# Kernel tuning notes

Measured on AMD Instinct MI355X. Metric: run time of the kernel, lower is better.

Reference implementation:

```python
import jax, jax.numpy as jnp
import numpy as np

B, L, HSIZE = 16, 512, 1024
H, D = 16, 64  # HHEAD = HSIZE/base, HBASE = 64

def setup_inputs() -> dict:
    key = jax.random.key(0)
    ks = jax.random.split(key, 10)
    inp = {
        'v': jax.random.normal(ks[0], (B, L, HSIZE), jnp.float32),
        'k': jax.random.normal(ks[1], (B, L, HSIZE), jnp.float32),
        'q': jax.random.normal(ks[2], (B, L, HSIZE), jnp.float32),
        'img_abs': jax.random.normal(ks[3], (B, L, HSIZE), jnp.float32),
        'Wv': jax.random.normal(ks[4], (HSIZE, HSIZE), jnp.float32) * 0.02,
        'Wk': jax.random.normal(ks[5], (HSIZE, HSIZE), jnp.float32) * 0.02,
        'Wq': jax.random.normal(ks[6], (HSIZE, HSIZE), jnp.float32) * 0.02,
        'Wm': jax.random.normal(ks[7], (HSIZE, HSIZE), jnp.float32) * 0.02,
        'abs_mask': jax.random.bernoulli(ks[8], 0.1, (B, 1, L, L)),
        'mask': jax.random.bernoulli(ks[9], 0.1, (B, 1, L, L)),
    }
    return inp

def reference(v, k, q, img_abs, Wv, Wk, Wq, Wm, abs_mask, mask):
    nb = q.shape[0]
    # Linear (no bias) then split heads: [B, L, HSIZE] -> [B, H, L, D]
    def heads(x):
        return x.reshape(nb, -1, H, D).transpose(0, 2, 1, 3)
    vh = heads(v @ Wv.T)
    kh = heads(k @ Wk.T)
    qh = heads(q @ Wq.T)
    ph = heads(img_abs)
    scale = 1.0 / jnp.sqrt(jnp.asarray(D, qh.dtype))
    # modulate: attention of q over positional features, residual-added to q
    s1 = jnp.einsum('bhqd,bhpd->bhqp', qh, ph) * scale
    s1 = jnp.where(abs_mask, jnp.asarray(-1e9, s1.dtype), s1)
    qh = qh + jnp.einsum('bhqp,bhpd->bhqd', jax.nn.softmax(s1, axis=-1), ph)
    # main attention (dropout = identity in eval mode)
    s2 = jnp.einsum('bhqd,bhkd->bhqk', qh, kh) * scale
    s2 = jnp.where(mask, jnp.asarray(-1e9, s2.dtype), s2)
    atted = jnp.einsum('bhqk,bhkd->bhqd', jax.nn.softmax(s2, axis=-1), vh)
    atted = atted.transpose(0, 2, 1, 3).reshape(nb, -1, H * D)
    return atted @ Wm.T
```

## Files before the change

kernel.cpp:

```cpp
#include <hip/hip_runtime.h>

typedef unsigned short u16;
typedef unsigned int u32;
typedef unsigned long long u64;
typedef __attribute__((ext_vector_type(8))) short short8;
typedef __attribute__((ext_vector_type(4))) float f32x4;
typedef __attribute__((ext_vector_type(4))) u32 u32x4;

#define NB 16
#define SL 512
#define HS 1024
#define NHEAD 16
#define HD 64
#define NTOKC (16L * 512 * 1024)
#define NWC   (1024L * 1024)
#define NMC   (16L * 512 * 512)

typedef const __attribute__((address_space(1))) u32* gas_t;
typedef __attribute__((address_space(3))) u32* las_t;

__device__ __forceinline__ void gld16(const u16* g, u16* l) {
  __builtin_amdgcn_global_load_lds((gas_t)g, (las_t)l, 16, 0, 0);
}

__device__ __forceinline__ u16 f2bf(float f) {
  union { float f; unsigned u; } c; c.f = f;
  unsigned r = c.u + 0x7FFFu + ((c.u >> 16) & 1u);
  return (u16)(r >> 16);
}
__device__ __forceinline__ float bf2f(u16 u) {
  union { float f; unsigned u; } c; c.u = ((unsigned)u) << 16;
  return c.f;
}

__global__ __launch_bounds__(256) void prep(
    const float* __restrict__ v, const float* __restrict__ k,
    const float* __restrict__ q, const float* __restrict__ img,
    const float* __restrict__ Wv, const float* __restrict__ Wk,
    const float* __restrict__ Wq, const float* __restrict__ Wm,
    const int* __restrict__ absm, const int* __restrict__ mask,
    u16* __restrict__ ovk, u16* __restrict__ xq, u16* __restrict__ pb,
    u16* __restrict__ w4, u64* __restrict__ bits) {
  const int y = blockIdx.y;
  const long bx = blockIdx.x;
  if (y < 4) {
    const float* in = y == 0 ? v : y == 1 ? k : y == 2 ? q : img;
    u16* out = y == 0 ? ovk : y == 1 ? ovk + NTOKC : y == 2 ? xq : pb;
    long i = (bx * 256 + threadIdx.x) * 4;
    float4 f = *(const float4*)(in + i);
    uint2 u;
    u.x = (unsigned)f2bf(f.x) | ((unsigned)f2bf(f.y) << 16);
    u.y = (unsigned)f2bf(f.z) | ((unsigned)f2bf(f.w) << 16);
    *(uint2*)(out + i) = u;
  } else if (y == 4) {
    if (bx >= 4096) return;
    long i = bx * 1024 + threadIdx.x * 4;
    int j = (int)(i >> 20);
    const float* in = j == 0 ? Wv : j == 1 ? Wk : j == 2 ? Wq : Wm;
    long off = i & (NWC - 1);
    float4 f = *(const float4*)(in + off);
    uint2 u;
    u.x = (unsigned)f2bf(f.x) | ((unsigned)f2bf(f.y) << 16);
    u.y = (unsigned)f2bf(f.z) | ((unsigned)f2bf(f.w) << 16);
    *(uint2*)(w4 + i) = u;
  } else {
#pragma unroll
    for (int rep = 0; rep < 4; ++rep) {
      long i = (bx * 4 + rep) * 256 + threadIdx.x;
      const int* m = (i >= NMC) ? mask : absm;
      long off = i & (NMC - 1);
      u64 bset = __ballot(m[off] != 0);
      if ((threadIdx.x & 63) == 0) bits[i >> 6] = bset;
    }
  }
}

__global__ __launch_bounds__(256) void gemm_p3(const u16* __restrict__ Avk,
                                               const u16* __restrict__ Aq,
                                               const u16* __restrict__ W4,
                                               u16* __restrict__ Cb) {
  __shared__ u16 As[128 * 64];
  __shared__ u16 Bs[128 * 64];
  const int tid = threadIdx.x;
  const int wave = tid >> 6, lane = tid & 63;
  const int quad = lane >> 4, l16 = lane & 15;
  const int l7 = l16 & 7;
  const int sel = blockIdx.x >> 6;
  const int row0 = (blockIdx.x & 63) * 128, col0 = blockIdx.y * 128;
  const int wm = (wave >> 1) * 64, wn = (wave & 1) * 64;
  const int lrow = lane >> 3;
  const int scb = (lane & 7) ^ lrow;
  const int K = HS, N = HS;

  const u16* A = (sel == 2) ? Aq : Avk + (long)sel * NTOKC;
  const u16* W = W4 + (long)sel * NWC;
  u16* C = Cb + (long)sel * NTOKC;

  f32x4 acc[4][4];
#pragma unroll
  for (int mt = 0; mt < 4; ++mt)
#pragma unroll
    for (int nt = 0; nt < 4; ++nt) acc[mt][nt] = (f32x4){0.f, 0.f, 0.f, 0.f};

  const u16* Ab = A + (long)row0 * K;
  const u16* Wb = W + (long)col0 * K;

  for (int k0 = 0; k0 < K; k0 += 64) {
    __syncthreads();
#pragma unroll
    for (int it = 0; it < 4; ++it) {
      int seg = wave * 4 + it;
      int r = seg * 8 + lrow;
      gld16(Ab + (long)r * K + k0 + scb * 8, As + seg * 512);
      gld16(Wb + (long)r * K + k0 + scb * 8, Bs + seg * 512);
    }
    __syncthreads();
#pragma unroll
    for (int kt = 0; kt < 2; ++kt) {
      short8 af[4], bw[4];
#pragma unroll
      for (int mt = 0; mt < 4; ++mt)
        af[mt] = *(const short8*)(As + (wm + mt * 16 + l16) * 64 +
                                  (((kt * 4 + quad) ^ l7) * 8));
#pragma unroll
      for (int nt = 0; nt < 4; ++nt)
        bw[nt] = *(const short8*)(Bs + (wn + nt * 16 + l16) * 64 +
                                  (((kt * 4 + quad) ^ l7) * 8));
#pragma unroll
      for (int mt = 0; mt < 4; ++mt)
#pragma unroll
        for (int nt = 0; nt < 4; ++nt)
          acc[mt][nt] = __builtin_amdgcn_mfma_f32_16x16x32_bf16(
              af[mt], bw[nt], acc[mt][nt], 0, 0, 0);
    }
  }
#pragma unroll
  for (int mt = 0; mt < 4; ++mt)
#pragma unroll
    for (int nt = 0; nt < 4; ++nt)
#pragma unroll
      for (int i = 0; i < 4; ++i) {
        long r = row0 + wm + mt * 16 + quad * 4 + i;
        long c = col0 + wn + nt * 16 + l16;
        C[r * N + c] = f2bf(acc[mt][nt][i]);
      }
}

__global__ __launch_bounds__(256) void gemm_f(const u16* __restrict__ A,
                                              const u16* __restrict__ W,
                                              float* __restrict__ C) {
  __shared__ u16 As[128 * 64];
  __shared__ u16 Bs[128 * 64];
  const int tid = threadIdx.x;
  const int wave = tid >> 6, lane = tid & 63;
  const int quad = lane >> 4, l16 = lane & 15;
  const int l7 = l16 & 7;
  const int row0 = blockIdx.x * 128, col0 = blockIdx.y * 128;
  const int wm = (wave >> 1) * 64, wn = (wave & 1) * 64;
  const int lrow = lane >> 3;
  const int scb = (lane & 7) ^ lrow;
  const int K = HS, N = HS;

  f32x4 acc[4][4];
#pragma unroll
  for (int mt = 0; mt < 4; ++mt)
#pragma unroll
    for (int nt = 0; nt < 4; ++nt) acc[mt][nt] = (f32x4){0.f, 0.f, 0.f, 0.f};

  const u16* Ab = A + (long)row0 * K;
  const u16* Wb = W + (long)col0 * K;

  for (int k0 = 0; k0 < K; k0 += 64) {
    __syncthreads();
#pragma unroll
    for (int it = 0; it < 4; ++it) {
      int seg = wave * 4 + it;
      int r = seg * 8 + lrow;
      gld16(Ab + (long)r * K + k0 + scb * 8, As + seg * 512);
      gld16(Wb + (long)r * K + k0 + scb * 8, Bs + seg * 512);
    }
    __syncthreads();
#pragma unroll
    for (int kt = 0; kt < 2; ++kt) {
      short8 af[4], bw[4];
#pragma unroll
      for (int mt = 0; mt < 4; ++mt)
        af[mt] = *(const short8*)(As + (wm + mt * 16 + l16) * 64 +
                                  (((kt * 4 + quad) ^ l7) * 8));
#pragma unroll
      for (int nt = 0; nt < 4; ++nt)
        bw[nt] = *(const short8*)(Bs + (wn + nt * 16 + l16) * 64 +
                                  (((kt * 4 + quad) ^ l7) * 8));
#pragma unroll
      for (int mt = 0; mt < 4; ++mt)
#pragma unroll
        for (int nt = 0; nt < 4; ++nt)
          acc[mt][nt] = __builtin_amdgcn_mfma_f32_16x16x32_bf16(
              af[mt], bw[nt], acc[mt][nt], 0, 0, 0);
    }
  }
#pragma unroll
  for (int mt = 0; mt < 4; ++mt)
#pragma unroll
    for (int nt = 0; nt < 4; ++nt)
#pragma unroll
      for (int i = 0; i < 4; ++i) {
        long r = row0 + wm + mt * 16 + quad * 4 + i;
        long c = col0 + wn + nt * 16 + l16;
        C[r * N + c] = acc[mt][nt][i];
      }
}

template <bool SAME>
__device__ __forceinline__ void attn_stage(
    const u16* __restrict__ Kb, const u16* __restrict__ Vb,
    const u64* __restrict__ Mb, int qrow, short8 qf[2], float& l_p,
    f32x4 o[4], u16 (*Ks)[72], u16 (*Vs)[72],
    int quad, int l16, int sr, int sds, int vcol) {
  uint4 kp = *(const uint4*)(Kb + (long)sr * HS + sds);
  uint4 vp;
  if (!SAME) vp = *(const uint4*)(Vb + (long)sr * HS + sds);
  for (int t = 0; t < 8; ++t) {
    __syncthreads();
    *(uint4*)&Ks[sr][sds] = kp;
    {
      union { uint4 q; u16 e[8]; } tv;
      tv.q = SAME ? kp : vp;
#pragma unroll
      for (int j = 0; j < 8; ++j) Vs[sds + j][vcol] = tv.e[j];
    }
    __syncthreads();
    if (t < 7) {
      kp = *(const uint4*)(Kb + (long)((t + 1) * 64 + sr) * HS + sds);
      if (!SAME)
        vp = *(const uint4*)(Vb + (long)((t + 1) * 64 + sr) * HS + sds);
    }
    const u64 mw = Mb[(long)qrow * 8 + t];
    f32x4 s[4];
#pragma unroll
    for (int nt = 0; nt < 4; ++nt) s[nt] = (f32x4){0.f, 0.f, 0.f, 0.f};
#pragma unroll
    for (int kt = 0; kt < 2; ++kt)
#pragma unroll
      for (int nt = 0; nt < 4; ++nt) {
        short8 ak = *(const short8*)&Ks[nt * 16 + l16][kt * 32 + quad * 8];
        s[nt] = __builtin_amdgcn_mfma_f32_16x16x32_bf16(ak, qf[kt], s[nt],
                                                        0, 0, 0);
      }
    u32 pk[8];
    float lp = 0.f;
#pragma unroll
    for (int nt = 0; nt < 4; ++nt) {
      const u32 mb = (u32)(mw >> (nt * 16 + quad * 4));
#pragma unroll
      for (int ih = 0; ih < 2; ++ih) {
        float p0 = (mb & (1u << (2 * ih))) ? 0.f
                                           : __expf(s[nt][2 * ih] * 0.125f);
        float p1 = (mb & (1u << (2 * ih + 1)))
                       ? 0.f
                       : __expf(s[nt][2 * ih + 1] * 0.125f);
        lp += p0 + p1;
        pk[nt * 2 + ih] = (u32)f2bf(p0) | ((u32)f2bf(p1) << 16);
      }
    }
    l_p += lp;
#pragma unroll
    for (int kt = 0; kt < 2; ++kt) {
      u32x4 av;
#pragma unroll
      for (int j2 = 0; j2 < 4; ++j2) {
        int src = ((quad & 1) * 2 + (j2 >> 1)) * 16 + l16;
        u32 vlo = (u32)__shfl((int)pk[(2 * kt) * 2 + (j2 & 1)], src, 64);
        u32 vhi = (u32)__shfl((int)pk[(2 * kt + 1) * 2 + (j2 & 1)], src, 64);
        av[j2] = (quad & 2) ? vhi : vlo;
      }
      union { u32x4 u; short8 s8; } cv;
      cv.u = av;
#pragma unroll
      for (int nt = 0; nt < 4; ++nt) {
        short8 bv = *(const short8*)&Vs[nt * 16 + l16]
                                      [(kt * 32 + quad * 8) ^ ((nt & 3) << 4)];
        o[nt] = __builtin_amdgcn_mfma_f32_16x16x32_bf16(cv.s8, bv, o[nt],
                                                        0, 0, 0);
      }
    }
  }
}

__global__ __launch_bounds__(512, 4) void attn_fused(
    const u16* __restrict__ Qp, const u16* __restrict__ Pbp,
    const u16* __restrict__ Kp, const u16* __restrict__ Vp,
    const u64* __restrict__ B0, const u64* __restrict__ B1,
    u16* __restrict__ Op) {
  __shared__ u16 KV[128][72];
  u16 (*Ks)[72] = KV;
  u16 (*Vs)[72] = KV + 64;
  const int tid = threadIdx.x;
  const int wave = tid >> 6, lane = tid & 63;
  const int quad = lane >> 4, l16 = lane & 15;
  const int qt = blockIdx.x, h = blockIdx.y, b = blockIdx.z;
  const int q0 = qt * 128;
  const long bs = (long)SL * HS;
  const u16* Qb = Qp + (long)b * bs + h * HD;
  const u16* Pb = Pbp + (long)b * bs + h * HD;
  const u16* Kb = Kp + (long)b * bs + h * HD;
  const u16* Vb = Vp + (long)b * bs + h * HD;
  const u64* M0 = B0 + (long)b * SL * 8;
  const u64* M1 = B1 + (long)b * SL * 8;
  const int sr = tid >> 3, sds = (tid & 7) * 8;
  const int vcol = sr ^ (((sds >> 4) & 3) << 4);
  const int qrow = q0 + wave * 16 + l16;

  short8 qf[2];
#pragma unroll
  for (int kt = 0; kt < 2; ++kt)
    qf[kt] = *(const short8*)(Qb + (long)qrow * HS + kt * 32 + quad * 8);

  float l_p = 0.f;
  f32x4 o[4];
#pragma unroll
  for (int nt = 0; nt < 4; ++nt) o[nt] = (f32x4){0.f, 0.f, 0.f, 0.f};

  attn_stage<true>(Pb, Pb, M0, qrow, qf, l_p, o, Ks, Vs, quad, l16, sr, sds,
                   vcol);

  {
    float rs = l_p;
    rs += __shfl_xor(rs, 16, 64);
    rs += __shfl_xor(rs, 32, 64);
    float inv = 1.f / rs;
    float invq[4];
#pragma unroll
    for (int i = 0; i < 4; ++i) invq[i] = __shfl(inv, quad * 4 + i, 64);
    __syncthreads();
#pragma unroll
    for (int i = 0; i < 4; ++i)
#pragma unroll
      for (int nt = 0; nt < 4; ++nt)
        KV[wave * 16 + quad * 4 + i][nt * 16 + l16] =
            f2bf(o[nt][i] * invq[i]);
#pragma unroll
    for (int kt = 0; kt < 2; ++kt) {
      short8 t8 = *(const short8*)&KV[wave * 16 + l16][kt * 32 + quad * 8];
#pragma unroll
      for (int j = 0; j < 8; ++j)
        qf[kt][j] = (short)f2bf(bf2f((u16)t8[j]) + bf2f((u16)qf[kt][j]));
    }
#pragma unroll
    for (int nt = 0; nt < 4; ++nt) o[nt] = (f32x4){0.f, 0.f, 0.f, 0.f};
    l_p = 0.f;
  }

  attn_stage<false>(Kb, Vb, M1, qrow, qf, l_p, o, Ks, Vs, quad, l16, sr, sds,
                    vcol);

  {
    float rs = l_p;
    rs += __shfl_xor(rs, 16, 64);
    rs += __shfl_xor(rs, 32, 64);
    float inv = 1.f / rs;
    float invq[4];
#pragma unroll
    for (int i = 0; i < 4; ++i) invq[i] = __shfl(inv, quad * 4 + i, 64);
    u16* Ob = Op + (long)b * bs + h * HD;
#pragma unroll
    for (int i = 0; i < 4; ++i) {
      int r = q0 + wave * 16 + quad * 4 + i;
#pragma unroll
      for (int nt = 0; nt < 4; ++nt)
        Ob[(long)r * HS + nt * 16 + l16] = f2bf(o[nt][i] * invq[i]);
    }
  }
}

extern "C" void kernel_launch(void* const* d_in, const int* in_sizes, int n_in,
                              void* d_out, int out_size, void* d_ws,
                              size_t ws_size, hipStream_t stream) {
  const float* v   = (const float*)d_in[0];
  const float* k   = (const float*)d_in[1];
  const float* q   = (const float*)d_in[2];
  const float* img = (const float*)d_in[3];
  const float* Wv  = (const float*)d_in[4];
  const float* Wk  = (const float*)d_in[5];
  const float* Wq  = (const float*)d_in[6];
  const float* Wm  = (const float*)d_in[7];
  const int* absm  = (const int*)d_in[8];
  const int* mask  = (const int*)d_in[9];
  float* out = (float*)d_out;

  const long NTOK = NTOKC;
  const long NW   = NWC;
  const long NM   = NMC;
  u16* ovk = (u16*)d_out;
  u16* ws  = (u16*)d_ws;
  u16* xq  = ws;
  u16* pb  = ws + 1 * NTOK;
  u16* vh  = ws + 2 * NTOK;
  u16* kh  = ws + 3 * NTOK;
  u16* qh  = ws + 4 * NTOK;
  u16* w4  = ws + 5 * NTOK;
  u64* bt0 = (u64*)(w4 + 4 * NW);
  u64* bt1 = bt0 + NM / 64;
  u16* att = xq;

  prep<<<dim3(8192, 6), 256, 0, stream>>>(v, k, q, img, Wv, Wk, Wq, Wm,
                                          absm, mask, ovk, xq, pb, w4, bt0);
  gemm_p3<<<dim3(192, 8), 256, 0, stream>>>(ovk, xq, w4, vh);
  attn_fused<<<dim3(SL / 128, NHEAD, NB), 512, 0, stream>>>(
      qh, pb, kh, vh, bt0, bt1, att);
  gemm_f<<<dim3(NB * SL / 128, HS / 128), 256, 0, stream>>>(att, w4 + 3 * NW,
                                                            out);
}
```

Baseline: 383.3 us.

## Double-buffer K/V shared tiles in attention and prefetch mask words

The attention stage now uses ping-pong shared-memory buffers for K and V, so the next tile is written while the current one is consumed, cutting one barrier per iteration. All eight mask words for the row are loaded up front, and the bf16 packing of probabilities uses a hardware packed-convert instruction. Shared memory per block doubles, which may reduce occupancy at 512 threads with 4 blocks per CU. An extra barrier is added between the two stages to protect the reused buffer.

```diff
diff --git a/kernel.cpp b/kernel.cpp
--- a/kernel.cpp
+++ b/kernel.cpp
@@ -31,6 +31,11 @@
 __device__ __forceinline__ float bf2f(u16 u) {
   union { float f; unsigned u; } c; c.u = ((unsigned)u) << 16;
   return c.f;
+}
+__device__ __forceinline__ u32 cvt_pk_bf16(float a, float b) {
+  u32 r;
+  asm("v_cvt_pk_bf16_f32 %0, %1, %2" : "=v"(r) : "v"(a), "v"(b));
+  return r;
 }
 
 __global__ __launch_bounds__(256) void prep(
@@ -217,25 +222,29 @@
     const u64* __restrict__ Mb, int qrow, short8 qf[2], float& l_p,
     f32x4 o[4], u16 (*Ks)[72], u16 (*Vs)[72],
     int quad, int l16, int sr, int sds, int vcol) {
+  u64 mall[8];
+#pragma unroll
+  for (int t = 0; t < 8; ++t) mall[t] = Mb[(long)qrow * 8 + t];
   uint4 kp = *(const uint4*)(Kb + (long)sr * HS + sds);
   uint4 vp;
   if (!SAME) vp = *(const uint4*)(Vb + (long)sr * HS + sds);
+  {
+    *(uint4*)&Ks[sr][sds] = kp;
+    union { uint4 q; u16 e[8]; } tv;
+    tv.q = SAME ? kp : vp;
+#pragma unroll
+    for (int j = 0; j < 8; ++j) Vs[sds + j][vcol] = tv.e[j];
+  }
+  __syncthreads();
   for (int t = 0; t < 8; ++t) {
-    __syncthreads();
-    *(uint4*)&Ks[sr][sds] = kp;
-    {
-      union { uint4 q; u16 e[8]; } tv;
-      tv.q = SAME ? kp : vp;
-#pragma unroll
-      for (int j = 0; j < 8; ++j) Vs[sds + j][vcol] = tv.e[j];
-    }
-    __syncthreads();
+    const int cur = t & 1;
     if (t < 7) {
       kp = *(const uint4*)(Kb + (long)((t + 1) * 64 + sr) * HS + sds);
       if (!SAME)
         vp = *(const uint4*)(Vb + (long)((t + 1) * 64 + sr) * HS + sds);
     }
-    const u64 mw = Mb[(long)qrow * 8 + t];
+    u16(*Kc)[72] = Ks + cur * 64;
+    u16(*Vc)[72] = Vs + cur * 64;
     f32x4 s[4];
 #pragma unroll
     for (int nt = 0; nt < 4; ++nt) s[nt] = (f32x4){0.f, 0.f, 0.f, 0.f};
@@ -243,10 +252,11 @@
     for (int kt = 0; kt < 2; ++kt)
 #pragma unroll
       for (int nt = 0; nt < 4; ++nt) {
-        short8 ak = *(const short8*)&Ks[nt * 16 + l16][kt * 32 + quad * 8];
+        short8 ak = *(const short8*)&Kc[nt * 16 + l16][kt * 32 + quad * 8];
         s[nt] = __builtin_amdgcn_mfma_f32_16x16x32_bf16(ak, qf[kt], s[nt],
                                                         0, 0, 0);
       }
+    const u64 mw = mall[t];
     u32 pk[8];
     float lp = 0.f;
 #pragma unroll
@@ -260,7 +270,7 @@
                        ? 0.f
                        : __expf(s[nt][2 * ih + 1] * 0.125f);
         lp += p0 + p1;
-        pk[nt * 2 + ih] = (u32)f2bf(p0) | ((u32)f2bf(p1) << 16);
+        pk[nt * 2 + ih] = cvt_pk_bf16(p0, p1);
       }
     }
     l_p += lp;
@@ -278,11 +288,21 @@
       cv.u = av;
 #pragma unroll
       for (int nt = 0; nt < 4; ++nt) {
-        short8 bv = *(const short8*)&Vs[nt * 16 + l16]
+        short8 bv = *(const short8*)&Vc[nt * 16 + l16]
                                       [(kt * 32 + quad * 8) ^ ((nt & 3) << 4)];
         o[nt] = __builtin_amdgcn_mfma_f32_16x16x32_bf16(cv.s8, bv, o[nt],
                                                         0, 0, 0);
       }
+    }
+    if (t < 7) {
+      u16(*Kn)[72] = Ks + (cur ^ 1) * 64;
+      u16(*Vn)[72] = Vs + (cur ^ 1) * 64;
+      *(uint4*)&Kn[sr][sds] = kp;
+      union { uint4 q; u16 e[8]; } tv;
+      tv.q = SAME ? kp : vp;
+#pragma unroll
+      for (int j = 0; j < 8; ++j) Vn[sds + j][vcol] = tv.e[j];
+      __syncthreads();
     }
   }
 }
@@ -292,9 +312,8 @@
     const u16* __restrict__ Kp, const u16* __restrict__ Vp,
     const u64* __restrict__ B0, const u64* __restrict__ B1,
     u16* __restrict__ Op) {
-  __shared__ u16 KV[128][72];
-  u16 (*Ks)[72] = KV;
-  u16 (*Vs)[72] = KV + 64;
+  __shared__ u16 Ks[128][72];
+  __shared__ u16 Vs[128][72];
   const int tid = threadIdx.x;
   const int wave = tid >> 6, lane = tid & 63;
   const int quad = lane >> 4, l16 = lane & 15;
@@ -337,11 +356,11 @@
     for (int i = 0; i < 4; ++i)
 #pragma unroll
       for (int nt = 0; nt < 4; ++nt)
-        KV[wave * 16 + quad * 4 + i][nt * 16 + l16] =
+        Ks[wave * 16 + quad * 4 + i][nt * 16 + l16] =
             f2bf(o[nt][i] * invq[i]);
 #pragma unroll
     for (int kt = 0; kt < 2; ++kt) {
-      short8 t8 = *(const short8*)&KV[wave * 16 + l16][kt * 32 + quad * 8];
+      short8 t8 = *(const short8*)&Ks[wave * 16 + l16][kt * 32 + quad * 8];
 #pragma unroll
       for (int j = 0; j < 8; ++j)
         qf[kt][j] = (short)f2bf(bf2f((u16)t8[j]) + bf2f((u16)qf[kt][j]));
@@ -349,6 +368,7 @@
 #pragma unroll
     for (int nt = 0; nt < 4; ++nt) o[nt] = (f32x4){0.f, 0.f, 0.f, 0.f};
     l_p = 0.f;
+    __syncthreads();
   }
 
   attn_stage<false>(Kb, Vb, M1, qrow, qf, l_p, o, Ks, Vs, quad, l16, sr, sds,
```

After: 381.7 us. About the same (-0.4%).
